# Optimization experiments

Measured on AMD Instinct MI355X. Metric: run time of the kernel, lower is better.

The kernel has to match this reference:

```python
import jax, jax.numpy as jnp
import numpy as np

B = 16          # events per minibatch
P = 4096        # generated points per event
Q = 4096        # ground-truth points per event
SPATIAL_SIZE = 256.0


def setup_inputs() -> dict:
    key = jax.random.key(0)
    k1, k2 = jax.random.split(key)
    points_gen = jax.random.normal(k1, (B * P, 3), dtype=jnp.float32)
    # batch ids: contiguous equal-size segments per event
    batch_gen = (jnp.arange(B * P, dtype=jnp.int32) // P).astype(jnp.int32)
    # label: col 0 = batch id, cols 1:4 = coords in [0, 256), col 4 = class label
    coords = jax.random.uniform(k2, (B * Q, 3), dtype=jnp.float32) * SPATIAL_SIZE
    batch_gt = (jnp.arange(B * Q, dtype=jnp.float32) // Q)
    cls = jnp.zeros((B * Q,), dtype=jnp.float32)
    label = jnp.concatenate([batch_gt[:, None], coords, cls[:, None]], axis=1)
    return {"points_gen": points_gen, "batch_gen": batch_gen, "label": label}


def _chamfer(x, y):
    # x: [P,3], y: [Q,3] -> symmetric Chamfer distance (squared Euclidean)
    x2 = jnp.sum(x * x, axis=-1)                      # [P]
    y2 = jnp.sum(y * y, axis=-1)                      # [Q]
    d = x2[:, None] + y2[None, :] - 2.0 * (x @ y.T)   # [P,Q]
    return jnp.mean(jnp.min(d, axis=1)) + jnp.mean(jnp.min(d, axis=0))


def reference(points_gen, batch_gen, label):
    half = SPATIAL_SIZE / 2.0
    points_gt = (label[:, 1:4] - half) / half          # normalize GT to [-1,1]
    # batch ids are contiguous equal segments -> masking == reshape
    x = points_gen.reshape(B, P, 3)
    y = points_gt.reshape(B, Q, 3)
    losses = jax.vmap(_chamfer)(x, y)                  # [B]
    loss = jnp.sum(losses) / B                         # loss / count
    return loss
```

## Files before the change

kernel.cpp:

```cpp
#include <hip/hip_runtime.h>


#define NB 16
#define NP 4096
#define NT 2048
#define THREADS 256
#define NROWS 131072
#define INV128 0.0078125f
#define FINF __int_as_float(0x7F800000)

typedef __attribute__((ext_vector_type(8)))  short bf16x8;
typedef __attribute__((ext_vector_type(16))) float f32x16;

__device__ __forceinline__ short bf16rne(float f) {
    unsigned u = __float_as_uint(f);
    return (short)((u + 0x7FFFu + ((u >> 16) & 1u)) >> 16);
}
__device__ __forceinline__ float bf2f(short s) {
    return __uint_as_float(((unsigned)(unsigned short)s) << 16);
}

__global__ __launch_bounds__(THREADS) void chamfer_kernel(const float* __restrict__ gen,
                                                          const float* __restrict__ label,
                                                          float* __restrict__ rowmins) {
    __shared__ short spack[NT * 8 + 1280];

    const int bid   = blockIdx.x;
    const int dir   = bid >> 9;
    const int b     = (bid >> 5) & 15;
    const int qpair = (bid >> 1) & 15;
    const int thalf = bid & 1;
    const int tid   = threadIdx.x;
    const int lane  = tid & 63;
    const int wave  = tid >> 6;
    const int base  = b * NP;
    const int tbase = base + thalf * NT;

    if (tid < 8) spack[NT * 8 + tid] = 0;

    #pragma unroll 4
    for (int k = 0; k < 8; ++k) {
        int j = tid + k * 256;
        float x, y, z;
        if (dir == 0) {
            const float* row = label + (size_t)(tbase + j) * 5;
            x = fmaf(row[1], INV128, -1.0f);
            y = fmaf(row[2], INV128, -1.0f);
            z = fmaf(row[3], INV128, -1.0f);
        } else {
            const float* g = gen + (size_t)(tbase + j) * 3;
            x = g[0]; y = g[1]; z = g[2];
        }
        float t2 = fmaf(x, x, fmaf(y, y, z * z));
        short xh = bf16rne(x), yh = bf16rne(y), zh = bf16rne(z);
        short xl = bf16rne(x - bf2f(xh));
        short yl = bf16rne(y - bf2f(yh));
        short zl2 = bf16rne(z - bf2f(zh));
        short th = bf16rne(t2);
        short tl = bf16rne(t2 - bf2f(th));
        bf16x8 v = {xh, yh, zh, xl, yl, zl2, th, tl};
        *(bf16x8*)(spack + j * 8) = v;
    }
    __syncthreads();

    const f32x16 zc = {};

    #pragma unroll 1
    for (int sub = 0; sub < 2; ++sub) {
        const int qrow = base + qpair * 256 + sub * 128 + wave * 32 + (lane & 31);
        float q2 = 0.0f;
        bf16x8 afrag = (bf16x8)(short)0;
        if (lane < 32) {
            float x, y, z;
            if (dir == 0) {
                const float* g = gen + (size_t)qrow * 3;
                x = g[0]; y = g[1]; z = g[2];
            } else {
                const float* row = label + (size_t)qrow * 5;
                x = fmaf(row[1], INV128, -1.0f);
                y = fmaf(row[2], INV128, -1.0f);
                z = fmaf(row[3], INV128, -1.0f);
            }
            q2 = fmaf(x, x, fmaf(y, y, z * z));
            short ax = bf16rne(-2.0f * x), ay = bf16rne(-2.0f * y), az = bf16rne(-2.0f * z);
            const short one = 0x3F80;
            bf16x8 a = {ax, ay, az, ax, ay, az, one, one};
            afrag = a;
        }

        float mn[16];
        #pragma unroll
        for (int r = 0; r < 16; ++r) mn[r] = FINF;

        const short* zl = spack + NT * 8;
        const short* p0 = (lane < 32) ? (spack + (lane & 31) * 8)       : zl;
        const short* p1 = (lane < 32) ? (spack + (lane & 31) * 8 + 256) : zl;
        const short* p2 = (lane < 32) ? (spack + (lane & 31) * 8 + 512) : zl;
        const short* p3 = (lane < 32) ? (spack + (lane & 31) * 8 + 768) : zl;
        const int step = (lane < 32) ? 1024 : 0;

        bf16x8 b0 = *(const bf16x8*)p0;
        bf16x8 b1 = *(const bf16x8*)p1;
        bf16x8 b2 = *(const bf16x8*)p2;
        bf16x8 b3 = *(const bf16x8*)p3;
        #pragma unroll 2
        for (int it = 0; it < 16; ++it) {
            p0 += step; p1 += step; p2 += step; p3 += step;
            bf16x8 n0 = *(const bf16x8*)p0;
            bf16x8 n1 = *(const bf16x8*)p1;
            bf16x8 n2 = *(const bf16x8*)p2;
            bf16x8 n3 = *(const bf16x8*)p3;
            f32x16 c0 = __builtin_amdgcn_mfma_f32_32x32x16_bf16(afrag, b0, zc, 0, 0, 0);
            f32x16 c1 = __builtin_amdgcn_mfma_f32_32x32x16_bf16(afrag, b1, zc, 0, 0, 0);
            f32x16 c2 = __builtin_amdgcn_mfma_f32_32x32x16_bf16(afrag, b2, zc, 0, 0, 0);
            f32x16 c3 = __builtin_amdgcn_mfma_f32_32x32x16_bf16(afrag, b3, zc, 0, 0, 0);
            #pragma unroll
            for (int r = 0; r < 16; ++r) {
                mn[r] = fminf(fminf(c0[r], c1[r]),
                              fminf(fminf(c2[r], c3[r]), mn[r]));
            }
            b0 = n0; b1 = n1; b2 = n2; b3 = n3;
        }

        #pragma unroll
        for (int m = 1; m <= 16; m <<= 1) {
            #pragma unroll
            for (int r = 0; r < 16; ++r)
                mn[r] = fminf(mn[r], __shfl_xor(mn[r], m, 64));
        }

        const int h4 = (lane >> 5) * 4;
        const int c  = lane & 31;
        const int row = (c & 3) + 8 * (c >> 2) + h4;
        float q2r = __shfl(q2, row & 31, 64);
        float v = mn[0];
        #pragma unroll
        for (int r = 1; r < 16; ++r) if (c == r) v = mn[r];
        if (c < 16) {
            size_t gidx = (size_t)thalf * NROWS
                        + (size_t)(((dir * NB + b) << 12) + qpair * 256 + sub * 128
                                   + wave * 32 + row);
            rowmins[gidx] = v + q2r;
        }
    }
}

__global__ __launch_bounds__(256) void minsum_kernel(const float* __restrict__ rowmins,
                                                     float* __restrict__ partial2) {
    const int tid = threadIdx.x;
    const int row = blockIdx.x * 256 + tid;
    float s = fminf(rowmins[row], rowmins[NROWS + row]);
    #pragma unroll
    for (int off = 32; off > 0; off >>= 1) s += __shfl_down(s, off, 64);
    __shared__ float w4[4];
    if ((tid & 63) == 0) w4[tid >> 6] = s;
    __syncthreads();
    if (tid == 0) partial2[blockIdx.x] = ((w4[0] + w4[1]) + (w4[2] + w4[3]));
}

__global__ __launch_bounds__(256) void reduce_kernel(const float* __restrict__ partial,
                                                     float* __restrict__ out) {
    int i = threadIdx.x;
    float s = partial[i] + partial[i + 256];
    #pragma unroll
    for (int off = 32; off > 0; off >>= 1) s += __shfl_down(s, off, 64);
    __shared__ float ws4[4];
    if ((i & 63) == 0) ws4[i >> 6] = s;
    __syncthreads();
    if (i == 0) out[0] = ((ws4[0] + ws4[1]) + (ws4[2] + ws4[3])) * (1.0f / 65536.0f);
}

extern "C" void kernel_launch(void* const* d_in, const int* in_sizes, int n_in,
                              void* d_out, int out_size, void* d_ws, size_t ws_size,
                              hipStream_t stream) {
    const float* gen   = (const float*)d_in[0];
    const float* label = (const float*)d_in[2];
    float* rowmins  = (float*)d_ws;
    float* partial2 = rowmins + 2 * NROWS;
    float* out = (float*)d_out;

    chamfer_kernel<<<1024, THREADS, 0, stream>>>(gen, label, rowmins);
    minsum_kernel<<<512, 256, 0, stream>>>(rowmins, partial2);
    reduce_kernel<<<1, 256, 0, stream>>>(partial2, out);
}
```

Baseline: 93.88 us.

## Compute both Chamfer directions from one distance matrix via shared-memory column atomics

Each block now computes each generated-to-GT distance tile once. It takes row minima as before and also folds column minima into shared memory with integer atomicMin on biased float bits. The query norm is folded into the MFMA by using the spare upper lanes, so the tile holds full distances. This halves the block count and the MFMA work, because the second direction no longer recomputes the transposed matrix. In exchange it adds per-iteration fold and atomic traffic to LDS, a larger workspace, and a combine kernel that reduces column minima across 16 row slices. The +1 bias relies on distances being non-negative for the int ordering.

After: 87.54 us. 1.07x faster.

```diff
diff --git a/kernel.cpp b/kernel.cpp
--- a/kernel.cpp
+++ b/kernel.cpp
@@ -5,7 +5,7 @@
 #define NP 4096
 #define NT 2048
 #define THREADS 256
-#define NROWS 131072
+#define NROWST 65536
 #define INV128 0.0078125f
 #define FINF __int_as_float(0x7F800000)
 
@@ -19,46 +19,51 @@
 __device__ __forceinline__ float bf2f(short s) {
     return __uint_as_float(((unsigned)(unsigned short)s) << 16);
 }
+__device__ __forceinline__ float fold16(const f32x16& c) {
+    float a = fminf(fminf(c[0], c[1]),  fminf(c[2],  c[3]));
+    float b = fminf(fminf(c[4], c[5]),  fminf(c[6],  c[7]));
+    float d = fminf(fminf(c[8], c[9]),  fminf(c[10], c[11]));
+    float e = fminf(fminf(c[12], c[13]), fminf(c[14], c[15]));
+    return fminf(fminf(a, b), fminf(d, e));
+}
 
 __global__ __launch_bounds__(THREADS) void chamfer_kernel(const float* __restrict__ gen,
                                                           const float* __restrict__ label,
-                                                          float* __restrict__ rowmins) {
+                                                          float* __restrict__ rowws,
+                                                          int* __restrict__ colws) {
     __shared__ short spack[NT * 8 + 1280];
-
-    const int bid   = blockIdx.x;
-    const int dir   = bid >> 9;
-    const int b     = (bid >> 5) & 15;
-    const int qpair = (bid >> 1) & 15;
-    const int thalf = bid & 1;
-    const int tid   = threadIdx.x;
-    const int lane  = tid & 63;
-    const int wave  = tid >> 6;
+    __shared__ int colmin[NT];
+
+    const int bid  = blockIdx.x;
+    const int b    = bid >> 5;
+    const int rs   = (bid >> 1) & 15;
+    const int cs   = bid & 1;
+    const int tid  = threadIdx.x;
+    const int lane = tid & 63;
+    const int wave = tid >> 6;
     const int base  = b * NP;
-    const int tbase = base + thalf * NT;
-
-    if (tid < 8) spack[NT * 8 + tid] = 0;
+    const int tbase = base + cs * NT;
+
+    if (tid < 8) spack[NT * 8 + tid] = (tid < 2) ? (short)0x3F80 : (short)0;
+
+    #pragma unroll
+    for (int k = 0; k < 8; ++k) colmin[tid + k * 256] = 0x7F800000;
 
     #pragma unroll 4
     for (int k = 0; k < 8; ++k) {
         int j = tid + k * 256;
-        float x, y, z;
-        if (dir == 0) {
-            const float* row = label + (size_t)(tbase + j) * 5;
-            x = fmaf(row[1], INV128, -1.0f);
-            y = fmaf(row[2], INV128, -1.0f);
-            z = fmaf(row[3], INV128, -1.0f);
-        } else {
-            const float* g = gen + (size_t)(tbase + j) * 3;
-            x = g[0]; y = g[1]; z = g[2];
-        }
+        const float* row = label + (size_t)(tbase + j) * 5;
+        float x = fmaf(row[1], INV128, -1.0f);
+        float y = fmaf(row[2], INV128, -1.0f);
+        float z = fmaf(row[3], INV128, -1.0f);
         float t2 = fmaf(x, x, fmaf(y, y, z * z));
         short xh = bf16rne(x), yh = bf16rne(y), zh = bf16rne(z);
         short xl = bf16rne(x - bf2f(xh));
         short yl = bf16rne(y - bf2f(yh));
-        short zl2 = bf16rne(z - bf2f(zh));
+        short zl = bf16rne(z - bf2f(zh));
         short th = bf16rne(t2);
         short tl = bf16rne(t2 - bf2f(th));
-        bf16x8 v = {xh, yh, zh, xl, yl, zl2, th, tl};
+        bf16x8 v = {xh, yh, zh, xl, yl, zl, th, tl};
         *(bf16x8*)(spack + j * 8) = v;
     }
     __syncthreads();
@@ -67,36 +72,32 @@
 
     #pragma unroll 1
     for (int sub = 0; sub < 2; ++sub) {
-        const int qrow = base + qpair * 256 + sub * 128 + wave * 32 + (lane & 31);
-        float q2 = 0.0f;
-        bf16x8 afrag = (bf16x8)(short)0;
+        const int qrow = base + rs * 256 + sub * 128 + wave * 32 + (lane & 31);
+        const float* g = gen + (size_t)qrow * 3;
+        float x = g[0], y = g[1], z = g[2];
+        float q2 = fmaf(x, x, fmaf(y, y, z * z));
+        bf16x8 afrag;
         if (lane < 32) {
-            float x, y, z;
-            if (dir == 0) {
-                const float* g = gen + (size_t)qrow * 3;
-                x = g[0]; y = g[1]; z = g[2];
-            } else {
-                const float* row = label + (size_t)qrow * 5;
-                x = fmaf(row[1], INV128, -1.0f);
-                y = fmaf(row[2], INV128, -1.0f);
-                z = fmaf(row[3], INV128, -1.0f);
-            }
-            q2 = fmaf(x, x, fmaf(y, y, z * z));
             short ax = bf16rne(-2.0f * x), ay = bf16rne(-2.0f * y), az = bf16rne(-2.0f * z);
             const short one = 0x3F80;
             bf16x8 a = {ax, ay, az, ax, ay, az, one, one};
             afrag = a;
+        } else {
+            short qh = bf16rne(q2);
+            short ql = bf16rne(q2 - bf2f(qh));
+            bf16x8 a = {qh, ql, 0, 0, 0, 0, 0, 0};
+            afrag = a;
         }
 
         float mn[16];
         #pragma unroll
         for (int r = 0; r < 16; ++r) mn[r] = FINF;
 
-        const short* zl = spack + NT * 8;
-        const short* p0 = (lane < 32) ? (spack + (lane & 31) * 8)       : zl;
-        const short* p1 = (lane < 32) ? (spack + (lane & 31) * 8 + 256) : zl;
-        const short* p2 = (lane < 32) ? (spack + (lane & 31) * 8 + 512) : zl;
-        const short* p3 = (lane < 32) ? (spack + (lane & 31) * 8 + 768) : zl;
+        const short* ol = spack + NT * 8;
+        const short* p0 = (lane < 32) ? (spack + (lane & 31) * 8)       : ol;
+        const short* p1 = (lane < 32) ? (spack + (lane & 31) * 8 + 256) : ol;
+        const short* p2 = (lane < 32) ? (spack + (lane & 31) * 8 + 512) : ol;
+        const short* p3 = (lane < 32) ? (spack + (lane & 31) * 8 + 768) : ol;
         const int step = (lane < 32) ? 1024 : 0;
 
         bf16x8 b0 = *(const bf16x8*)p0;
@@ -119,6 +120,11 @@
                 mn[r] = fminf(fminf(c0[r], c1[r]),
                               fminf(fminf(c2[r], c3[r]), mn[r]));
             }
+            const int cb = it * 128 + (lane & 31);
+            atomicMin(&colmin[cb],       __float_as_int(fold16(c0) + 1.0f));
+            atomicMin(&colmin[cb + 32],  __float_as_int(fold16(c1) + 1.0f));
+            atomicMin(&colmin[cb + 64],  __float_as_int(fold16(c2) + 1.0f));
+            atomicMin(&colmin[cb + 96],  __float_as_int(fold16(c3) + 1.0f));
             b0 = n0; b1 = n1; b2 = n2; b3 = n3;
         }
 
@@ -132,30 +138,43 @@
         const int h4 = (lane >> 5) * 4;
         const int c  = lane & 31;
         const int row = (c & 3) + 8 * (c >> 2) + h4;
-        float q2r = __shfl(q2, row & 31, 64);
         float v = mn[0];
         #pragma unroll
         for (int r = 1; r < 16; ++r) if (c == r) v = mn[r];
-        if (c < 16) {
-            size_t gidx = (size_t)thalf * NROWS
-                        + (size_t)(((dir * NB + b) << 12) + qpair * 256 + sub * 128
-                                   + wave * 32 + row);
-            rowmins[gidx] = v + q2r;
-        }
+        if (c < 16)
+            rowws[cs * NROWST + base + rs * 256 + sub * 128 + wave * 32 + row] = v;
     }
-}
-
-__global__ __launch_bounds__(256) void minsum_kernel(const float* __restrict__ rowmins,
-                                                     float* __restrict__ partial2) {
+
+    __syncthreads();
+    const int cwbase = ((b * 2 + cs) * 16 + rs) * NT;
+    #pragma unroll
+    for (int k = 0; k < 8; ++k)
+        colws[cwbase + tid + k * 256] = colmin[tid + k * 256];
+}
+
+__global__ __launch_bounds__(256) void combine_kernel(const float* __restrict__ rowws,
+                                                      const int* __restrict__ colws,
+                                                      float* __restrict__ partial2) {
     const int tid = threadIdx.x;
-    const int row = blockIdx.x * 256 + tid;
-    float s = fminf(rowmins[row], rowmins[NROWS + row]);
+    const int bid = blockIdx.x;
+    float s;
+    if (bid < 256) {
+        int row = bid * 256 + tid;
+        s = fminf(rowws[row], rowws[NROWST + row]);
+    } else {
+        int gidx = (bid - 256) * 256 + tid;
+        const int* cw = colws + (gidx >> 11) * (16 * NT) + (gidx & (NT - 1));
+        int k = cw[0];
+        #pragma unroll
+        for (int r2 = 1; r2 < 16; ++r2) k = min(k, cw[r2 * NT]);
+        s = __int_as_float(k) - 1.0f;
+    }
     #pragma unroll
     for (int off = 32; off > 0; off >>= 1) s += __shfl_down(s, off, 64);
     __shared__ float w4[4];
     if ((tid & 63) == 0) w4[tid >> 6] = s;
     __syncthreads();
-    if (tid == 0) partial2[blockIdx.x] = ((w4[0] + w4[1]) + (w4[2] + w4[3]));
+    if (tid == 0) partial2[bid] = (w4[0] + w4[1]) + (w4[2] + w4[3]);
 }
 
 __global__ __launch_bounds__(256) void reduce_kernel(const float* __restrict__ partial,
@@ -175,11 +194,12 @@
                               hipStream_t stream) {
     const float* gen   = (const float*)d_in[0];
     const float* label = (const float*)d_in[2];
-    float* rowmins  = (float*)d_ws;
-    float* partial2 = rowmins + 2 * NROWS;
+    float* rowws    = (float*)d_ws;
+    int*   colws    = (int*)d_ws + 2 * NROWST;
+    float* partial2 = (float*)d_ws + 2 * NROWST + NB * 2 * 16 * NT;
     float* out = (float*)d_out;
 
-    chamfer_kernel<<<1024, THREADS, 0, stream>>>(gen, label, rowmins);
-    minsum_kernel<<<512, 256, 0, stream>>>(rowmins, partial2);
+    chamfer_kernel<<<512, THREADS, 0, stream>>>(gen, label, rowws, colws);
+    combine_kernel<<<512, 256, 0, stream>>>(rowws, colws, partial2);
     reduce_kernel<<<1, 256, 0, stream>>>(partial2, out);
 }
```
